# Performance work log

Measured on AMD Instinct MI355X. Metric: run time of the kernel, lower is better.

## Reference

```python
import jax, jax.numpy as jnp
import numpy as np

NUM_INPUTS, NUM_HIDDEN, NUM_OUTPUTS = 512, 1024, 35
T, B = 100, 512
N_HID_LAYERS = 4  # number of hidden Leaky layers (num_layers)
SLOPE = 25.0      # snntorch surrogate.fast_sigmoid default slope
BETA, THR = 0.95, 1.0


@jax.custom_vjp
def spike(x):
    # Heaviside forward, fast-sigmoid surrogate backward
    return (x > 0).astype(x.dtype)

def _spike_fwd(x):
    return (x > 0).astype(x.dtype), x

def _spike_bwd(x, g):
    return (g / (SLOPE * jnp.abs(x) + 1.0) ** 2,)

spike.defvjp(_spike_fwd, _spike_bwd)


def leaky(x, mem, beta, thr):
    # snntorch Leaky, reset_mechanism='subtract':
    # reset computed from PREVIOUS mem (detached), then decay+input, then fire
    reset = jax.lax.stop_gradient((mem - thr > 0).astype(x.dtype))
    mem = jnp.clip(beta, 0.0, 1.0) * mem + x - reset * thr
    spk = spike(mem - thr)
    return spk, mem


def setup_inputs() -> dict:
    key = jax.random.key(0)
    ks = jax.random.split(key, 8)
    data = jax.random.normal(ks[0], (T, B, NUM_INPUTS), dtype=jnp.float32)
    s_in = 1.0 / np.sqrt(NUM_INPUTS)
    s_h = 1.0 / np.sqrt(NUM_HIDDEN)
    W_in = jax.random.uniform(ks[1], (NUM_HIDDEN, NUM_INPUTS), minval=-s_in, maxval=s_in, dtype=jnp.float32)
    b_in = jax.random.uniform(ks[2], (NUM_HIDDEN,), minval=-s_in, maxval=s_in, dtype=jnp.float32)
    W_h = jax.random.uniform(ks[3], (N_HID_LAYERS - 1, NUM_HIDDEN, NUM_HIDDEN), minval=-s_h, maxval=s_h, dtype=jnp.float32)
    b_h = jax.random.uniform(ks[4], (N_HID_LAYERS - 1, NUM_HIDDEN), minval=-s_h, maxval=s_h, dtype=jnp.float32)
    W_out = jax.random.uniform(ks[5], (NUM_OUTPUTS, NUM_HIDDEN), minval=-s_h, maxval=s_h, dtype=jnp.float32)
    b_out = jax.random.uniform(ks[6], (NUM_OUTPUTS,), minval=-s_h, maxval=s_h, dtype=jnp.float32)
    # learn_beta/learn_threshold: each Leaky holds its own (identically initialized) params
    beta_h = jnp.full((N_HID_LAYERS, NUM_HIDDEN), BETA, dtype=jnp.float32)
    thr_h = jnp.full((N_HID_LAYERS, NUM_HIDDEN), THR, dtype=jnp.float32)
    beta_o = jnp.full((NUM_OUTPUTS,), BETA, dtype=jnp.float32)
    thr_o = jnp.full((NUM_OUTPUTS,), THR, dtype=jnp.float32)
    return {"data": data, "W_in": W_in, "b_in": b_in, "W_h": W_h, "b_h": b_h,
            "W_out": W_out, "b_out": b_out, "beta_h": beta_h, "thr_h": thr_h,
            "beta_o": beta_o, "thr_o": thr_o, "timestep": 100}


def reference(data, W_in, b_in, W_h, b_h, W_out, b_out, beta_h, thr_h, beta_o, thr_o, timestep):
    n_hid = beta_h.shape[0]
    Bsz = data.shape[1]

    def step(mems, x_t):
        new_mems = []
        x = x_t @ W_in.T + b_in
        x, m = leaky(x, mems[0], beta_h[0], thr_h[0])
        new_mems.append(m)
        for i in range(n_hid - 1):
            z = x @ W_h[i].T + b_h[i]
            x, m = leaky(z, mems[i + 1], beta_h[i + 1], thr_h[i + 1])
            new_mems.append(m)
        z = x @ W_out.T + b_out
        spk, m = leaky(z, mems[n_hid], beta_o, thr_o)
        new_mems.append(m)
        return tuple(new_mems), spk

    mems0 = tuple([jnp.zeros((Bsz, NUM_HIDDEN), dtype=data.dtype) for _ in range(n_hid)]
                  + [jnp.zeros((Bsz, NUM_OUTPUTS), dtype=data.dtype)])
    _, spk_rec = jax.lax.scan(step, mems0, data[:timestep])
    return spk_rec  # [T, B, num_outputs]
```

## Files before the change

kernel.cpp:

```cpp
#include <hip/hip_runtime.h>
#include <hip/hip_bf16.h>


#define NB 512
#define NH 1024
#define NI 512
#define NO 35
#define TT 100
#define NT 8
#define BITFRAME 16384

typedef __bf16 bf16x8 __attribute__((ext_vector_type(8)));
typedef float f32x4 __attribute__((ext_vector_type(4)));

__device__ __forceinline__ size_t tiled_off(int row, int k, int KT) {
    return ((size_t)((row >> 4) * KT + (k >> 5)) * 64
            + (row & 15) + (((k >> 3) & 3) << 4)) * 8 + (k & 7);
}

__device__ __forceinline__ void leaky_upd(float zin, float mprev, float be, float th,
                                          float& mnew, float& spk) {
    float rs = (mprev - th > 0.0f) ? th : 0.0f;
    float bc = fminf(fmaxf(be, 0.0f), 1.0f);
    mnew = bc * mprev + zin - rs;
    spk  = (mnew - th > 0.0f) ? 1.0f : 0.0f;
}

#define WS_MEM123   0u
#define WS_MEM0     6291456u
#define WS_MEMO     8388608u
#define WS_FLAGS    8486912u
#define WS_GEN      8487936u
#define WS_RING0    8488192u
#define WS_RING1    9536768u
#define WS_RING2    10585344u
#define WS_RING3    11633920u
#define WS_WT       12682496u
#define WS_WIT      31556864u
#define WS_WOT      34702592u
#define WS_Z0       34997504u
#define STEP_BYTES  2097152u

__global__ __launch_bounds__(256)
void split_weights(const float* __restrict__ W_h, __bf16* __restrict__ Wt) {
    const int id = blockIdx.x * 256 + threadIdx.x;
    const int layer = id >> 17;
    const int rem = id & 131071;
    const int n = rem >> 7;
    const int k0 = (rem & 127) << 3;
    const float* src = W_h + ((size_t)layer * NH + n) * NH + k0;
    __bf16* dst = Wt + (size_t)layer * 3 * NH * NH;
    const size_t PS = (size_t)NH * NH;
    const size_t off = tiled_off(n, k0, 32);
    bf16x8 p1, p2, p3;
    #pragma unroll
    for (int j = 0; j < 8; ++j) {
        float w = src[j];
        __bf16 a = (__bf16)w;  float r1 = w - (float)a;
        __bf16 b = (__bf16)r1; float r2 = r1 - (float)b;
        __bf16 c = (__bf16)r2;
        p1[j] = a; p2[j] = b; p3[j] = c;
    }
    *reinterpret_cast<bf16x8*>(dst + 0 * PS + off) = p1;
    *reinterpret_cast<bf16x8*>(dst + 1 * PS + off) = p2;
    *reinterpret_cast<bf16x8*>(dst + 2 * PS + off) = p3;
}

__global__ __launch_bounds__(256)
void split_win(const float* __restrict__ W_in, __bf16* __restrict__ Wi_t) {
    const int id = blockIdx.x * 256 + threadIdx.x;
    const int n = id >> 6;
    const int k0 = (id & 63) << 3;
    const float* src = W_in + (size_t)n * NI + k0;
    const size_t PS = (size_t)NH * NI;
    const size_t off = tiled_off(n, k0, 16);
    bf16x8 p1, p2, p3;
    #pragma unroll
    for (int j = 0; j < 8; ++j) {
        float w = src[j];
        __bf16 a = (__bf16)w;  float r1 = w - (float)a;
        __bf16 b = (__bf16)r1; float r2 = r1 - (float)b;
        __bf16 c = (__bf16)r2;
        p1[j] = a; p2[j] = b; p3[j] = c;
    }
    *reinterpret_cast<bf16x8*>(Wi_t + 0 * PS + off) = p1;
    *reinterpret_cast<bf16x8*>(Wi_t + 1 * PS + off) = p2;
    *reinterpret_cast<bf16x8*>(Wi_t + 2 * PS + off) = p3;
}

__global__ __launch_bounds__(256)
void split_wout(const float* __restrict__ W_out, __bf16* __restrict__ Wo_t) {
    const int id = blockIdx.x * 256 + threadIdx.x;
    if (id >= 48 * 128) return;
    const int o = id >> 7;
    const int k0 = (id & 127) << 3;
    const size_t PS = (size_t)48 * NH;
    const size_t off = tiled_off(o, k0, 32);
    bf16x8 p1 = {}, p2 = {}, p3 = {};
    if (o < NO) {
        const float* src = W_out + (size_t)o * NH + k0;
        #pragma unroll
        for (int j = 0; j < 8; ++j) {
            float w = src[j];
            __bf16 a = (__bf16)w;  float r1 = w - (float)a;
            __bf16 b = (__bf16)r1; float r2 = r1 - (float)b;
            __bf16 c = (__bf16)r2;
            p1[j] = a; p2[j] = b; p3[j] = c;
        }
    }
    *reinterpret_cast<bf16x8*>(Wo_t + 0 * PS + off) = p1;
    *reinterpret_cast<bf16x8*>(Wo_t + 1 * PS + off) = p2;
    *reinterpret_cast<bf16x8*>(Wo_t + 2 * PS + off) = p3;
}

__global__ __launch_bounds__(256)
void z0_gemm(const float* __restrict__ X,
             const __bf16* __restrict__ Wi_t,
             const float* __restrict__ bias,
             float* __restrict__ Z0)
{
    const int tid = threadIdx.x;
    const int lane = tid & 63;
    const int w = tid >> 6;
    const int wm = w >> 1, wn = w & 1;
    const int m_base = blockIdx.y * 64 + wm * 32;
    const int n_base = blockIdx.x * 64 + wn * 32;
    const size_t PS = (size_t)NH * NI;

    f32x4 acc[2][2] = {};
    bf16x8 a1[2], a2[2], a3[2];

    for (int kt = 0; kt < 16; ++kt) {
        #pragma unroll
        for (int mt = 0; mt < 2; ++mt) {
            const int row = m_base + mt * 16 + (lane & 15);
            const float* src = X + (size_t)row * NI + kt * 32 + ((lane >> 4) << 3);
            float4 v0 = *reinterpret_cast<const float4*>(src);
            float4 v1 = *reinterpret_cast<const float4*>(src + 4);
            float xv[8] = {v0.x, v0.y, v0.z, v0.w, v1.x, v1.y, v1.z, v1.w};
            #pragma unroll
            for (int j = 0; j < 8; ++j) {
                float x = xv[j];
                __bf16 h1 = (__bf16)x;  float r1 = x - (float)h1;
                __bf16 h2 = (__bf16)r1; float r2 = r1 - (float)h2;
                __bf16 h3 = (__bf16)r2;
                a1[mt][j] = h1; a2[mt][j] = h2; a3[mt][j] = h3;
            }
        }
        #pragma unroll
        for (int nt = 0; nt < 2; ++nt) {
            const size_t bo = ((size_t)(((n_base >> 4) + nt) * 16 + kt) * 64 + lane) * 8;
            bf16x8 b1 = *reinterpret_cast<const bf16x8*>(Wi_t + bo);
            bf16x8 b2 = *reinterpret_cast<const bf16x8*>(Wi_t + PS + bo);
            bf16x8 b3 = *reinterpret_cast<const bf16x8*>(Wi_t + 2 * PS + bo);
            #pragma unroll
            for (int mt = 0; mt < 2; ++mt) {
                f32x4 A = acc[mt][nt];
                A = __builtin_amdgcn_mfma_f32_16x16x32_bf16(a1[mt], b1, A, 0, 0, 0);
                A = __builtin_amdgcn_mfma_f32_16x16x32_bf16(a1[mt], b2, A, 0, 0, 0);
                A = __builtin_amdgcn_mfma_f32_16x16x32_bf16(a2[mt], b1, A, 0, 0, 0);
                A = __builtin_amdgcn_mfma_f32_16x16x32_bf16(a2[mt], b2, A, 0, 0, 0);
                A = __builtin_amdgcn_mfma_f32_16x16x32_bf16(a1[mt], b3, A, 0, 0, 0);
                A = __builtin_amdgcn_mfma_f32_16x16x32_bf16(a3[mt], b1, A, 0, 0, 0);
                acc[mt][nt] = A;
            }
        }
    }

    const int c = lane & 15;
    const int r0 = (lane >> 4) * 4;
    #pragma unroll
    for (int nt = 0; nt < 2; ++nt) {
        const int n = n_base + nt * 16 + c;
        const float bi = bias[n];
        #pragma unroll
        for (int mt = 0; mt < 2; ++mt) {
            #pragma unroll
            for (int r = 0; r < 4; ++r) {
                const int m = m_base + mt * 16 + r0 + r;
                const int tl = m >> 9, b = m & 511;
                Z0[(size_t)tl * (NB * NH) + tiled_off(b, n, 32)] = acc[mt][nt][r] + bi;
            }
        }
    }
}

__device__ __forceinline__ void gridbar(int* flags, int* gen, int target) {
    __syncthreads();
    if (threadIdx.x == 0) {
        __builtin_amdgcn_fence(__ATOMIC_RELEASE, "agent");
        __hip_atomic_store(&flags[blockIdx.x], target, __ATOMIC_RELAXED, __HIP_MEMORY_SCOPE_AGENT);
    }
    if (blockIdx.x == 0) {
        if (threadIdx.x < 64) {
            const int l = threadIdx.x;
            for (;;) {
                int v0 = __hip_atomic_load(&flags[l],       __ATOMIC_RELAXED, __HIP_MEMORY_SCOPE_AGENT);
                int v1 = __hip_atomic_load(&flags[l + 64],  __ATOMIC_RELAXED, __HIP_MEMORY_SCOPE_AGENT);
                int v2 = __hip_atomic_load(&flags[l + 128], __ATOMIC_RELAXED, __HIP_MEMORY_SCOPE_AGENT);
                int v3 = __hip_atomic_load(&flags[l + 192], __ATOMIC_RELAXED, __HIP_MEMORY_SCOPE_AGENT);
                int mn = min(min(v0, v1), min(v2, v3));
                if (__all(mn >= target)) break;
                __builtin_amdgcn_s_sleep(1);
            }
        }
        __syncthreads();
        if (threadIdx.x == 0) {
            __builtin_amdgcn_fence(__ATOMIC_ACQ_REL, "agent");
            __hip_atomic_store(gen, target, __ATOMIC_RELAXED, __HIP_MEMORY_SCOPE_AGENT);
        }
    } else if (threadIdx.x == 0) {
        while (__hip_atomic_load(gen, __ATOMIC_RELAXED, __HIP_MEMORY_SCOPE_AGENT) < target)
            __builtin_amdgcn_s_sleep(2);
    }
    __syncthreads();
    __builtin_amdgcn_fence(__ATOMIC_ACQUIRE, "agent");
}

template<int NS>
__device__ __forceinline__ void hidden_run(
    const unsigned int* const* Xp, unsigned short* const* Yp,
    const __bf16* Wldsp, const unsigned long long* lutp, const __bf16* W3,
    int cs, int rh, int w, int lane,
    float (&memr)[2][2][4], const float (&bi)[2], const float (&be)[2],
    const float (&th)[2])
{
    const int row = lane & 15;
    const int sh = (lane >> 4) * 8;
    f32x4 acc[NS][2][2] = {};
    unsigned int bw[NS][2];
    bf16x8 w3f[2];

    #pragma unroll
    for (int q = 0; q < NS; ++q)
        #pragma unroll
        for (int i = 0; i < 2; ++i)
            bw[q][i] = Xp[q][((rh * 16 + w * 2 + i) * 32) * 16 + row];
    #pragma unroll
    for (int nt = 0; nt < 2; ++nt)
        w3f[nt] = *reinterpret_cast<const bf16x8*>(W3 + (size_t)(cs * 2 + nt) * 16384 + lane * 8);

    for (int kt = 0; kt < 32; ++kt) {
        unsigned int nb[NS][2];
        bf16x8 nw3[2];
        if (kt < 31) {
            #pragma unroll
            for (int q = 0; q < NS; ++q)
                #pragma unroll
                for (int i = 0; i < 2; ++i)
                    nb[q][i] = Xp[q][((rh * 16 + w * 2 + i) * 32 + kt + 1) * 16 + row];
            #pragma unroll
            for (int nt = 0; nt < 2; ++nt)
                nw3[nt] = *reinterpret_cast<const bf16x8*>(
                    W3 + (size_t)(cs * 2 + nt) * 16384 + (size_t)(kt + 1) * 512 + lane * 8);
        }
        const int lo = kt * 512 + lane * 8;
        bf16x8 b10 = *reinterpret_cast<const bf16x8*>(Wldsp + 0 * 16384 + lo);
        bf16x8 b11 = *reinterpret_cast<const bf16x8*>(Wldsp + 1 * 16384 + lo);
        bf16x8 b20 = *reinterpret_cast<const bf16x8*>(Wldsp + 2 * 16384 + lo);
        bf16x8 b21 = *reinterpret_cast<const bf16x8*>(Wldsp + 3 * 16384 + lo);

        #pragma unroll
        for (int q = 0; q < NS; ++q) {
            #pragma unroll
            for (int i = 0; i < 2; ++i) {
                unsigned int by = (bw[q][i] >> sh) & 0xffu;
                union { unsigned long long u[2]; bf16x8 v; } a;
                a.u[0] = lutp[by & 15u];
                a.u[1] = lutp[by >> 4];
                acc[q][i][0] = __builtin_amdgcn_mfma_f32_16x16x32_bf16(a.v, b10, acc[q][i][0], 0, 0, 0);
                acc[q][i][1] = __builtin_amdgcn_mfma_f32_16x16x32_bf16(a.v, b11, acc[q][i][1], 0, 0, 0);
                acc[q][i][0] = __builtin_amdgcn_mfma_f32_16x16x32_bf16(a.v, b20, acc[q][i][0], 0, 0, 0);
                acc[q][i][1] = __builtin_amdgcn_mfma_f32_16x16x32_bf16(a.v, b21, acc[q][i][1], 0, 0, 0);
                acc[q][i][0] = __builtin_amdgcn_mfma_f32_16x16x32_bf16(a.v, w3f[0], acc[q][i][0], 0, 0, 0);
                acc[q][i][1] = __builtin_amdgcn_mfma_f32_16x16x32_bf16(a.v, w3f[1], acc[q][i][1], 0, 0, 0);
            }
        }
        if (kt < 31) {
            #pragma unroll
            for (int q = 0; q < NS; ++q) { bw[q][0] = nb[q][0]; bw[q][1] = nb[q][1]; }
            w3f[0] = nw3[0]; w3f[1] = nw3[1];
        }
    }

    #pragma unroll
    for (int q = 0; q < NS; ++q) {
        #pragma unroll
        for (int i = 0; i < 2; ++i) {
            #pragma unroll
            for (int nt = 0; nt < 2; ++nt) {
                #pragma unroll
                for (int r = 0; r < 4; ++r) {
                    float mn, sp;
                    leaky_upd(acc[q][i][nt][r] + bi[nt], memr[i][nt][r], be[nt], th[nt], mn, sp);
                    memr[i][nt][r] = mn;
                    unsigned long long bal = __ballot(sp != 0.0f);
                    if ((lane & 15) == 0) {
                        const int rr = (lane >> 4) * 4 + r;
                        Yp[q][(((rh * 16 + w * 2 + i) * 32 + cs) * 16 + rr) * 2 + nt] =
                            (unsigned short)((bal >> ((lane >> 4) * 16)) & 0xFFFFu);
                    }
                }
            }
        }
    }
}

__global__ __launch_bounds__(512, 1)
void snn_pipe(const float* __restrict__ Z0,
              const __bf16* __restrict__ Wt,
              const __bf16* __restrict__ Wo_t,
              const float* __restrict__ b_h,
              const float* __restrict__ b_out,
              const float* __restrict__ beta_h,
              const float* __restrict__ thr_h,
              const float* __restrict__ beta_o,
              const float* __restrict__ thr_o,
              float* __restrict__ mem123,
              float* __restrict__ mem0_g,
              float* __restrict__ memo_g,
              unsigned int* __restrict__ ring0, unsigned int* __restrict__ ring1,
              unsigned int* __restrict__ ring2, unsigned int* __restrict__ ring3,
              float* __restrict__ out,
              int* __restrict__ flags, int* __restrict__ gen,
              int t0, int tc)
{
    __shared__ __bf16 Wlds[4 * 32 * 512];
    __shared__ unsigned long long lut[16];

    const int blk  = blockIdx.x;
    const int tid  = threadIdx.x;
    const int lane = tid & 63;
    const int w    = tid >> 6;

    if (tid < 16) {
        unsigned int lo = ((tid & 1) ? 0x3F80u : 0u) | ((tid & 2) ? 0x3F800000u : 0u);
        unsigned int hi = ((tid & 4) ? 0x3F80u : 0u) | ((tid & 8) ? 0x3F800000u : 0u);
        lut[tid] = ((unsigned long long)hi << 32) | lo;
    }

    const int G = (tc + NT - 1) / NT;

    if (blk < 192) {
        const int ell = blk >> 6;
        const int cs  = (blk & 63) >> 1;
        const int rh  = blk & 1;
        {
            const __bf16* Wbase = Wt + (size_t)ell * 3 * (NH * NH);
            #pragma unroll
            for (int p = 0; p < 2; ++p)
                #pragma unroll
                for (int nt = 0; nt < 2; ++nt) {
                    const bf16x8* src = reinterpret_cast<const bf16x8*>(
                        Wbase + (size_t)p * (NH * NH) + (size_t)(cs * 2 + nt) * 16384);
                    bf16x8* dst = reinterpret_cast<bf16x8*>(Wlds + (p * 2 + nt) * 16384);
                    for (int i = tid; i < 2048; i += 512) dst[i] = src[i];
                }
        }
        const __bf16* W3 = Wt + (size_t)ell * 3 * (NH * NH) + 2 * (size_t)(NH * NH);

        const int c = lane & 15;
        const int r0v = (lane >> 4) * 4;
        float* memg = mem123 + (size_t)ell * (NB * NH);
        float bi[2], be[2], th[2];
        #pragma unroll
        for (int nt = 0; nt < 2; ++nt) {
            const int n = cs * 32 + nt * 16 + c;
            bi[nt] = b_h[ell * NH + n];
            be[nt] = beta_h[(ell + 1) * NH + n];
            th[nt] = thr_h[(ell + 1) * NH + n];
        }
        float memr[2][2][4];
        #pragma unroll
        for (int i = 0; i < 2; ++i)
            #pragma unroll
            for (int nt = 0; nt < 2; ++nt)
                #pragma unroll
                for (int r = 0; r < 4; ++r)
                    memr[i][nt][r] = memg[(size_t)(rh * 256 + (w * 2 + i) * 16 + r0v + r) * NH
                                          + cs * 32 + nt * 16 + c];

        const unsigned int* rin = (ell == 0) ? ring0 : (ell == 1) ? ring1 : ring2;
        unsigned int* rout      = (ell == 0) ? ring1 : (ell == 1) ? ring2 : ring3;

        __syncthreads();

        for (int p = 0; p < G + 4; ++p) {
            const int g = p - 1 - ell;
            if (g >= 0 && g < G) {
                const int sbase = g * NT;
                const int send  = (sbase + NT < tc) ? sbase + NT : tc;
                const int slot0 = (g & 1) * NT;
                int s = sbase;
                while (s < send) {
                    const int base = slot0 + (s - sbase);
                    const unsigned int* Xp[4];
                    unsigned short* Yp[4];
                    if (send - s >= 4) {
                        #pragma unroll
                        for (int q = 0; q < 4; ++q) {
                            Xp[q] = rin + (size_t)(base + q) * BITFRAME;
                            Yp[q] = (unsigned short*)(rout + (size_t)(base + q) * BITFRAME);
                        }
                        hidden_run<4>(Xp, Yp, Wlds, lut, W3, cs, rh, w, lane, memr, bi, be, th);
                        s += 4;
                    } else {
                        Xp[0] = rin + (size_t)base * BITFRAME;
                        Yp[0] = (unsigned short*)(rout + (size_t)base * BITFRAME);
                        hidden_run<1>(Xp, Yp, Wlds, lut, W3, cs, rh, w, lane, memr, bi, be, th);
                        s += 1;
                    }
                }
            }
            gridbar(flags, gen, p + 1);
        }

        #pragma unroll
        for (int i = 0; i < 2; ++i)
            #pragma unroll
            for (int nt = 0; nt < 2; ++nt)
                #pragma unroll
                for (int r = 0; r < 4; ++r)
                    memg[(size_t)(rh * 256 + (w * 2 + i) * 16 + r0v + r) * NH
                         + cs * 32 + nt * 16 + c] = memr[i][nt][r];
    } else {
        const int zt   = (blk - 192) * 512 + tid;
        const int wi   = zt >> 1;
        const int byt0 = (zt & 1) * 2;
        const int mtb  = wi >> 9;
        const int ktb  = (wi >> 4) & 31;
        const int rowb = wi & 15;
        const int i0   = (mtb * 32 + ktb) * 512 + rowb * 8 + byt0 * 128;
        const int n8   = ktb * 32 + byt0 * 8;

        float m0[16], be0[16], th0[16];
        #pragma unroll
        for (int j = 0; j < 8; ++j) {
            m0[j]      = mem0_g[i0 + j];
            m0[8 + j]  = mem0_g[i0 + 128 + j];
            be0[j]     = beta_h[n8 + j];
            be0[8 + j] = beta_h[n8 + 8 + j];
            th0[j]     = thr_h[n8 + j];
            th0[8 + j] = thr_h[n8 + 8 + j];
        }

        const bool outw = (blk < 224) && (w < 3);
        const int omt = blk - 192;
        const int ont = w;
        const int c = lane & 15, r0v = (lane >> 4) * 4;
        const int row = lane & 15, sh2 = (lane >> 4) * 8;
        const int oo = ont * 16 + c;
        const size_t OPS = (size_t)48 * NH;
        float mo[4] = {0.f, 0.f, 0.f, 0.f};
        float obi = 0.f, obe = 0.f, oth = 1.f;
        if (outw && oo < NO) {
            obi = b_out[oo]; obe = beta_o[oo]; oth = thr_o[oo];
            #pragma unroll
            for (int r = 0; r < 4; ++r) mo[r] = memo_g[(omt * 16 + r0v + r) * NO + oo];
        }

        __syncthreads();

        for (int p = 0; p < G + 4; ++p) {
            if (p < G) {
                const int sbase = p * NT;
                const int send  = (sbase + NT < tc) ? sbase + NT : tc;
                const int slot0 = (p & 1) * NT;
                for (int s = sbase; s < send; ++s) {
                    const float* zs = Z0 + (size_t)s * (NB * NH);
                    unsigned short* dsth =
                        (unsigned short*)(ring0 + (size_t)(slot0 + s - sbase) * BITFRAME);
                    float4 za = *reinterpret_cast<const float4*>(zs + i0);
                    float4 zb = *reinterpret_cast<const float4*>(zs + i0 + 4);
                    float4 zc = *reinterpret_cast<const float4*>(zs + i0 + 128);
                    float4 zd = *reinterpret_cast<const float4*>(zs + i0 + 132);
                    float zv[16] = {za.x, za.y, za.z, za.w, zb.x, zb.y, zb.z, zb.w,
                                    zc.x, zc.y, zc.z, zc.w, zd.x, zd.y, zd.z, zd.w};
                    unsigned int bits = 0;
                    #pragma unroll
                    for (int j = 0; j < 16; ++j) {
                        float mn, sp;
                        leaky_upd(zv[j], m0[j], be0[j], th0[j], mn, sp);
                        m0[j] = mn;
                        bits |= (sp != 0.0f ? 1u : 0u) << j;
                    }
                    dsth[zt] = (unsigned short)bits;
                }
            }
            if (outw) {
                const int go = p - 4;
                if (go >= 0 && go < G) {
                    const int sbase = go * NT;
                    const int send  = (sbase + NT < tc) ? sbase + NT : tc;
                    const int slot0 = (go & 1) * NT;
                    for (int s = sbase; s < send; ++s) {
                        const unsigned int* Xw =
                            ring3 + (size_t)(slot0 + s - sbase) * BITFRAME;
                        f32x4 acc = {};
                        for (int kt = 0; kt < 32; ++kt) {
                            unsigned int by = (Xw[(omt * 32 + kt) * 16 + row] >> sh2) & 0xffu;
                            union { unsigned long long u[2]; bf16x8 v; } a;
                            a.u[0] = lut[by & 15u];
                            a.u[1] = lut[by >> 4];
                            const size_t bo = ((size_t)(ont * 32 + kt) * 64 + lane) * 8;
                            bf16x8 q1 = *reinterpret_cast<const bf16x8*>(Wo_t + bo);
                            bf16x8 q2 = *reinterpret_cast<const bf16x8*>(Wo_t + OPS + bo);
                            bf16x8 q3 = *reinterpret_cast<const bf16x8*>(Wo_t + 2 * OPS + bo);
                            acc = __builtin_amdgcn_mfma_f32_16x16x32_bf16(a.v, q1, acc, 0, 0, 0);
                            acc = __builtin_amdgcn_mfma_f32_16x16x32_bf16(a.v, q2, acc, 0, 0, 0);
                            acc = __builtin_amdgcn_mfma_f32_16x16x32_bf16(a.v, q3, acc, 0, 0, 0);
                        }
                        if (oo < NO) {
                            #pragma unroll
                            for (int r = 0; r < 4; ++r) {
                                float mn, sp;
                                leaky_upd(acc[r] + obi, mo[r], obe, oth, mn, sp);
                                mo[r] = mn;
                                out[((size_t)(t0 + s) * NB + omt * 16 + r0v + r) * NO + oo] = sp;
                            }
                        }
                    }
                }
            }
            gridbar(flags, gen, p + 1);
        }

        #pragma unroll
        for (int j = 0; j < 8; ++j) {
            mem0_g[i0 + j]       = m0[j];
            mem0_g[i0 + 128 + j] = m0[8 + j];
        }
        if (outw && oo < NO) {
            #pragma unroll
            for (int r = 0; r < 4; ++r) memo_g[(omt * 16 + r0v + r) * NO + oo] = mo[r];
        }
    }
}

extern "C" void kernel_launch(void* const* d_in, const int* in_sizes, int n_in,
                              void* d_out, int out_size, void* d_ws, size_t ws_size,
                              hipStream_t stream) {
    const float* data   = (const float*)d_in[0];
    const float* W_in   = (const float*)d_in[1];
    const float* b_in   = (const float*)d_in[2];
    const float* W_h    = (const float*)d_in[3];
    const float* b_h    = (const float*)d_in[4];
    const float* W_out  = (const float*)d_in[5];
    const float* b_out  = (const float*)d_in[6];
    const float* beta_h = (const float*)d_in[7];
    const float* thr_h  = (const float*)d_in[8];
    const float* beta_o = (const float*)d_in[9];
    const float* thr_o  = (const float*)d_in[10];
    float* out = (float*)d_out;

    char* ws = (char*)d_ws;
    float*        mem123 = (float*)(ws + WS_MEM123);
    float*        mem0_g = (float*)(ws + WS_MEM0);
    float*        memo_g = (float*)(ws + WS_MEMO);
    int*          flags  = (int*)(ws + WS_FLAGS);
    int*          gen    = (int*)(ws + WS_GEN);
    unsigned int* ring0  = (unsigned int*)(ws + WS_RING0);
    unsigned int* ring1  = (unsigned int*)(ws + WS_RING1);
    unsigned int* ring2  = (unsigned int*)(ws + WS_RING2);
    unsigned int* ring3  = (unsigned int*)(ws + WS_RING3);
    __bf16*       Wt     = (__bf16*)(ws + WS_WT);
    __bf16*       Wi_t   = (__bf16*)(ws + WS_WIT);
    __bf16*       Wo_t   = (__bf16*)(ws + WS_WOT);
    float*        Z0     = (float*)(ws + WS_Z0);

    size_t avail = (ws_size > WS_Z0) ? (ws_size - WS_Z0) / STEP_BYTES : 1;
    int Tc = (int)(avail < 1 ? 1 : (avail > TT ? TT : avail));

    hipMemsetAsync(ws, 0, WS_FLAGS, stream);
    split_weights<<<dim3(1536), dim3(256), 0, stream>>>(W_h, Wt);
    split_win<<<dim3(256), dim3(256), 0, stream>>>(W_in, Wi_t);
    split_wout<<<dim3(24), dim3(256), 0, stream>>>(W_out, Wo_t);

    for (int t0c = 0; t0c < TT; t0c += Tc) {
        const int tcc = (TT - t0c < Tc) ? (TT - t0c) : Tc;
        z0_gemm<<<dim3(NH / 64, tcc * (NB / 64)), dim3(256), 0, stream>>>(
            data + (size_t)t0c * NB * NI, Wi_t, b_in, Z0);
        hipMemsetAsync(ws + WS_FLAGS, 0, 1280, stream);
        snn_pipe<<<dim3(256), dim3(512), 0, stream>>>(
            Z0, Wt, Wo_t, b_h, b_out, beta_h, thr_h, beta_o, thr_o,
            mem123, mem0_g, memo_g, ring0, ring1, ring2, ring3, out,
            flags, gen, t0c, tcc);
    }
}
```

Baseline: 1.850 ms.

## Double steps per pipeline stage, split layer-0 blocks, prefetch z0 GEMM inputs

Raises the number of timesteps per pipeline stage from 8 to 16, which halves the number of grid barriers and enlarges the ring buffers, so the workspace offsets move. The layer-0 leaky/bit-packing work now runs in its own blocks (blk>=224), separate from the output-layer blocks, with each thread packing 32 neurons into a full 32-bit word. The z0 GEMM gets register double-buffering that loads the next K-tile of X while the current one runs. Larger stages add pipeline fill/drain latency, and the new block split only works if the launch grid has enough blocks for it.

```diff
diff --git a/kernel.cpp b/kernel.cpp
--- a/kernel.cpp
+++ b/kernel.cpp
@@ -7,7 +7,7 @@
 #define NI 512
 #define NO 35
 #define TT 100
-#define NT 8
+#define NT 16
 #define BITFRAME 16384
 
 typedef __bf16 bf16x8 __attribute__((ext_vector_type(8)));
@@ -32,13 +32,13 @@
 #define WS_FLAGS    8486912u
 #define WS_GEN      8487936u
 #define WS_RING0    8488192u
-#define WS_RING1    9536768u
-#define WS_RING2    10585344u
-#define WS_RING3    11633920u
-#define WS_WT       12682496u
-#define WS_WIT      31556864u
-#define WS_WOT      34702592u
-#define WS_Z0       34997504u
+#define WS_RING1    10585344u
+#define WS_RING2    12682496u
+#define WS_RING3    14779648u
+#define WS_WT       16876800u
+#define WS_WIT      35751168u
+#define WS_WOT      38896896u
+#define WS_Z0       39191808u
 #define STEP_BYTES  2097152u
 
 __global__ __launch_bounds__(256)
@@ -128,16 +128,32 @@
     const size_t PS = (size_t)NH * NI;
 
     f32x4 acc[2][2] = {};
-    bf16x8 a1[2], a2[2], a3[2];
+    const float* asrc[2];
+    #pragma unroll
+    for (int mt = 0; mt < 2; ++mt)
+        asrc[mt] = X + (size_t)(m_base + mt * 16 + (lane & 15)) * NI + ((lane >> 4) << 3);
+
+    float4 c0[2], c1[2];
+    #pragma unroll
+    for (int mt = 0; mt < 2; ++mt) {
+        c0[mt] = *reinterpret_cast<const float4*>(asrc[mt]);
+        c1[mt] = *reinterpret_cast<const float4*>(asrc[mt] + 4);
+    }
 
     for (int kt = 0; kt < 16; ++kt) {
+        float4 n0[2], n1[2];
+        if (kt < 15) {
+            #pragma unroll
+            for (int mt = 0; mt < 2; ++mt) {
+                n0[mt] = *reinterpret_cast<const float4*>(asrc[mt] + (kt + 1) * 32);
+                n1[mt] = *reinterpret_cast<const float4*>(asrc[mt] + (kt + 1) * 32 + 4);
+            }
+        }
+        bf16x8 a1[2], a2[2], a3[2];
         #pragma unroll
         for (int mt = 0; mt < 2; ++mt) {
-            const int row = m_base + mt * 16 + (lane & 15);
-            const float* src = X + (size_t)row * NI + kt * 32 + ((lane >> 4) << 3);
-            float4 v0 = *reinterpret_cast<const float4*>(src);
-            float4 v1 = *reinterpret_cast<const float4*>(src + 4);
-            float xv[8] = {v0.x, v0.y, v0.z, v0.w, v1.x, v1.y, v1.z, v1.w};
+            float xv[8] = {c0[mt].x, c0[mt].y, c0[mt].z, c0[mt].w,
+                           c1[mt].x, c1[mt].y, c1[mt].z, c1[mt].w};
             #pragma unroll
             for (int j = 0; j < 8; ++j) {
                 float x = xv[j];
@@ -164,6 +180,10 @@
                 A = __builtin_amdgcn_mfma_f32_16x16x32_bf16(a3[mt], b1, A, 0, 0, 0);
                 acc[mt][nt] = A;
             }
+        }
+        if (kt < 15) {
+            #pragma unroll
+            for (int mt = 0; mt < 2; ++mt) { c0[mt] = n0[mt]; c1[mt] = n1[mt]; }
         }
     }
 
@@ -423,28 +443,8 @@
                 for (int r = 0; r < 4; ++r)
                     memg[(size_t)(rh * 256 + (w * 2 + i) * 16 + r0v + r) * NH
                          + cs * 32 + nt * 16 + c] = memr[i][nt][r];
-    } else {
-        const int zt   = (blk - 192) * 512 + tid;
-        const int wi   = zt >> 1;
-        const int byt0 = (zt & 1) * 2;
-        const int mtb  = wi >> 9;
-        const int ktb  = (wi >> 4) & 31;
-        const int rowb = wi & 15;
-        const int i0   = (mtb * 32 + ktb) * 512 + rowb * 8 + byt0 * 128;
-        const int n8   = ktb * 32 + byt0 * 8;
-
-        float m0[16], be0[16], th0[16];
-        #pragma unroll
-        for (int j = 0; j < 8; ++j) {
-            m0[j]      = mem0_g[i0 + j];
-            m0[8 + j]  = mem0_g[i0 + 128 + j];
-            be0[j]     = beta_h[n8 + j];
-            be0[8 + j] = beta_h[n8 + 8 + j];
-            th0[j]     = thr_h[n8 + j];
-            th0[8 + j] = thr_h[n8 + 8 + j];
-        }
-
-        const bool outw = (blk < 224) && (w < 3);
+    } else if (blk < 224) {
+        const bool outw = (w < 3);
         const int omt = blk - 192;
         const int ont = w;
         const int c = lane & 15, r0v = (lane >> 4) * 4;
@@ -458,35 +458,9 @@
             #pragma unroll
             for (int r = 0; r < 4; ++r) mo[r] = memo_g[(omt * 16 + r0v + r) * NO + oo];
         }
-
         __syncthreads();
 
         for (int p = 0; p < G + 4; ++p) {
-            if (p < G) {
-                const int sbase = p * NT;
-                const int send  = (sbase + NT < tc) ? sbase + NT : tc;
-                const int slot0 = (p & 1) * NT;
-                for (int s = sbase; s < send; ++s) {
-                    const float* zs = Z0 + (size_t)s * (NB * NH);
-                    unsigned short* dsth =
-                        (unsigned short*)(ring0 + (size_t)(slot0 + s - sbase) * BITFRAME);
-                    float4 za = *reinterpret_cast<const float4*>(zs + i0);
-                    float4 zb = *reinterpret_cast<const float4*>(zs + i0 + 4);
-                    float4 zc = *reinterpret_cast<const float4*>(zs + i0 + 128);
-                    float4 zd = *reinterpret_cast<const float4*>(zs + i0 + 132);
-                    float zv[16] = {za.x, za.y, za.z, za.w, zb.x, zb.y, zb.z, zb.w,
-                                    zc.x, zc.y, zc.z, zc.w, zd.x, zd.y, zd.z, zd.w};
-                    unsigned int bits = 0;
-                    #pragma unroll
-                    for (int j = 0; j < 16; ++j) {
-                        float mn, sp;
-                        leaky_upd(zv[j], m0[j], be0[j], th0[j], mn, sp);
-                        m0[j] = mn;
-                        bits |= (sp != 0.0f ? 1u : 0u) << j;
-                    }
-                    dsth[zt] = (unsigned short)bits;
-                }
-            }
             if (outw) {
                 const int go = p - 4;
                 if (go >= 0 && go < G) {
@@ -525,15 +499,61 @@
             gridbar(flags, gen, p + 1);
         }
 
-        #pragma unroll
-        for (int j = 0; j < 8; ++j) {
-            mem0_g[i0 + j]       = m0[j];
-            mem0_g[i0 + 128 + j] = m0[8 + j];
-        }
         if (outw && oo < NO) {
             #pragma unroll
             for (int r = 0; r < 4; ++r) memo_g[(omt * 16 + r0v + r) * NO + oo] = mo[r];
         }
+    } else {
+        const int wi   = (blk - 224) * 512 + tid;
+        const int mtb  = wi >> 9;
+        const int ktb  = (wi >> 4) & 31;
+        const int rowb = wi & 15;
+        const int i0   = (mtb * 32 + ktb) * 512 + rowb * 8;
+
+        float m0[32], be0[32], th0[32];
+        #pragma unroll
+        for (int byt = 0; byt < 4; ++byt)
+            #pragma unroll
+            for (int j = 0; j < 8; ++j) {
+                m0[byt * 8 + j]  = mem0_g[i0 + byt * 128 + j];
+                be0[byt * 8 + j] = beta_h[ktb * 32 + byt * 8 + j];
+                th0[byt * 8 + j] = thr_h[ktb * 32 + byt * 8 + j];
+            }
+        __syncthreads();
+
+        for (int p = 0; p < G + 4; ++p) {
+            if (p < G) {
+                const int sbase = p * NT;
+                const int send  = (sbase + NT < tc) ? sbase + NT : tc;
+                const int slot0 = (p & 1) * NT;
+                for (int s = sbase; s < send; ++s) {
+                    const float* zs = Z0 + (size_t)s * (NB * NH) + i0;
+                    float4 zv[8];
+                    #pragma unroll
+                    for (int byt = 0; byt < 4; ++byt) {
+                        zv[byt * 2]     = *reinterpret_cast<const float4*>(zs + byt * 128);
+                        zv[byt * 2 + 1] = *reinterpret_cast<const float4*>(zs + byt * 128 + 4);
+                    }
+                    unsigned int bits = 0;
+                    #pragma unroll
+                    for (int e = 0; e < 32; ++e) {
+                        float z = reinterpret_cast<const float*>(zv)[e];
+                        float mn, sp;
+                        leaky_upd(z, m0[e], be0[e], th0[e], mn, sp);
+                        m0[e] = mn;
+                        bits |= (sp != 0.0f ? 1u : 0u) << e;
+                    }
+                    ring0[(size_t)(slot0 + s - sbase) * BITFRAME + wi] = bits;
+                }
+            }
+            gridbar(flags, gen, p + 1);
+        }
+
+        #pragma unroll
+        for (int byt = 0; byt < 4; ++byt)
+            #pragma unroll
+            for (int j = 0; j < 8; ++j)
+                mem0_g[i0 + byt * 128 + j] = m0[byt * 8 + j];
     }
 }
 
```

Result: slower. 1.893 ms (+2.3%).
